# Kernel optimization log

Hardware: AMD Instinct MI355X
Metric: run time of the kernel (lower is better)

## Reference

```python
import jax, jax.numpy as jnp
import numpy as np

N_NODES = 50000
IN_FEATS, HID_FEATS, OUT_FEATS, HEADS = 128, 32, 64, 4
NEG_SLOPE = 0.2
EPS = 1e-16


def gat_conv(x, src, dst, W, att_src, att_dst, bias, heads, out_ch, concat):
    """PyG-style GATConv. src/dst: [E] (self-loops already included).
    W: [in, heads*out_ch]; att_src/att_dst: [heads, out_ch]; bias: [heads*out_ch] or [out_ch].
    """
    n = x.shape[0]
    xw = (x @ W).reshape(n, heads, out_ch)                     # [N,H,C]
    a_src = (xw * att_src).sum(-1)                             # [N,H]
    a_dst = (xw * att_dst).sum(-1)                             # [N,H]
    e = jax.nn.leaky_relu(a_src[src] + a_dst[dst], NEG_SLOPE)  # [E,H]
    # segment softmax over incoming edges of each destination node
    m = jax.ops.segment_max(e, dst, num_segments=n)
    e = jnp.exp(e - m[dst])
    denom = jax.ops.segment_sum(e, dst, num_segments=n)
    alpha = e / (denom[dst] + EPS)                             # [E,H]
    out = jax.ops.segment_sum(alpha[:, :, None] * xw[src], dst, num_segments=n)  # [N,H,C]
    out = out.reshape(n, heads * out_ch) if concat else out.mean(axis=1)
    return out + bias


def setup_inputs() -> dict:
    key = jax.random.key(0)
    ks = jax.random.split(key, 10)
    E = 1600000
    x = jax.random.normal(ks[0], (N_NODES, IN_FEATS), dtype=jnp.float32)
    edge_index = jax.random.randint(ks[1], (2, E), 0, N_NODES, dtype=jnp.int64)
    s1 = 1.0 / np.sqrt(IN_FEATS)
    W1 = jax.random.uniform(ks[2], (IN_FEATS, HEADS * HID_FEATS), jnp.float32, -s1, s1)
    att_src1 = jax.random.normal(ks[3], (HEADS, HID_FEATS), dtype=jnp.float32) * 0.1
    att_dst1 = jax.random.normal(ks[4], (HEADS, HID_FEATS), dtype=jnp.float32) * 0.1
    b1 = jnp.zeros((HEADS * HID_FEATS,), jnp.float32)
    s2 = 1.0 / np.sqrt(HEADS * HID_FEATS)
    W2 = jax.random.uniform(ks[5], (HEADS * HID_FEATS, OUT_FEATS), jnp.float32, -s2, s2)
    att_src2 = jax.random.normal(ks[6], (1, OUT_FEATS), dtype=jnp.float32) * 0.1
    att_dst2 = jax.random.normal(ks[7], (1, OUT_FEATS), dtype=jnp.float32) * 0.1
    b2 = jnp.zeros((OUT_FEATS,), jnp.float32)
    return {"x": x, "edge_index": edge_index, "W1": W1, "att_src1": att_src1,
            "att_dst1": att_dst1, "b1": b1, "W2": W2, "att_src2": att_src2,
            "att_dst2": att_dst2, "b2": b2}


def reference(x, edge_index, W1, att_src1, att_dst1, b1, W2, att_src2, att_dst2, b2):
    n = x.shape[0]
    loops = jnp.arange(n, dtype=edge_index.dtype)
    src = jnp.concatenate([edge_index[0], loops])
    dst = jnp.concatenate([edge_index[1], loops])
    h = gat_conv(x, src, dst, W1, att_src1, att_dst1, b1, HEADS, HID_FEATS, True)
    h = jax.nn.elu(h)
    h = gat_conv(h, src, dst, W2, att_src2, att_dst2, b2, 1, OUT_FEATS, False)
    return h.mean(axis=0)
```

## Files before the change

### kernel.cpp

```cpp
#include <hip/hip_runtime.h>
#include <math.h>

#define N_NODES 50000
#define E_RAW   1600000
#define TE      (E_RAW + N_NODES)
#define TEP     (TE + 8 * N_NODES)
#define F_IN    128
#define H1      4
#define F1      128
#define F2      64
#define NEG_SLOPE 0.2f
#define EPS_F   1e-16f
#define XPAD    136

#define NBINS   196
#define NBLK_A  128
#define EPB     ((TE + NBLK_A - 1) / NBLK_A)
#define MM_BLOCKS (N_NODES / 16)

__device__ __forceinline__ float lrelu(float v) { return v > 0.f ? v : NEG_SLOPE * v; }

typedef float vf2 __attribute__((ext_vector_type(2)));
typedef short short8 __attribute__((ext_vector_type(8)));
typedef float f32x4 __attribute__((ext_vector_type(4)));

__device__ __forceinline__ unsigned short f2bf(float f) {
    unsigned u = __float_as_uint(f);
    return (unsigned short)((u + 0x7fffu + ((u >> 16) & 1u)) >> 16);
}
__device__ __forceinline__ float bf2f(unsigned short s) {
    return __uint_as_float(((unsigned)s) << 16);
}
__device__ __forceinline__ unsigned char f2fp8(float f) {
    int p = __builtin_amdgcn_cvt_pk_fp8_f32(f, f, 0, false);
    return (unsigned char)(p & 0xff);
}
__device__ __forceinline__ vf2 fp8pair2f(int u) {
    return __builtin_amdgcn_cvt_pk_f32_fp8(u, false);
}

__global__ __launch_bounds__(256) void k_prep(const float* __restrict__ W1,
                                              const float* __restrict__ W2,
                                              unsigned short* __restrict__ w1t,
                                              unsigned short* __restrict__ w2t) {
    int idx = blockIdx.x * 256 + threadIdx.x;
    if (idx < 16384) {
        int c = idx >> 7, k = idx & 127;
        w1t[idx] = f2bf(W1[k * F1 + c]);
    } else {
        int j = idx - 16384;
        int c = j >> 7, k = j & 127;
        w2t[j] = f2bf(W2[k * F2 + c]);
    }
}

__global__ __launch_bounds__(256) void k_l1_mm_hist(
    const float* __restrict__ x, const unsigned short* __restrict__ w1t,
    const float* __restrict__ atts, const float* __restrict__ attd,
    unsigned char* __restrict__ xwf8, float* __restrict__ a1s, float* __restrict__ a1d,
    const int* __restrict__ ei, int* __restrict__ cnt) {
    __shared__ __align__(16) unsigned short wls[F1 * XPAD];
    __shared__ __align__(16) unsigned short xs[16 * XPAD];
    const int t = threadIdx.x;
    if (blockIdx.x >= MM_BLOCKS) {
        int* hist = (int*)wls;
        const int blk = blockIdx.x - MM_BLOCKS;
        for (int i = t; i < NBINS; i += 256) hist[i] = 0;
        __syncthreads();
        const int e0 = blk * EPB, e1 = min(TE, e0 + EPB);
        for (int e = e0 + t; e < e1; e += 256) {
            int d = (e < E_RAW) ? ei[E_RAW + e] : (e - E_RAW);
            atomicAdd(&hist[d >> 8], 1);
        }
        __syncthreads();
        for (int i = t; i < NBINS; i += 256) cnt[i * NBLK_A + blk] = hist[i];
        return;
    }
    const int n0 = blockIdx.x * 16;
    {
        const float4* src = (const float4*)(x + (size_t)n0 * F_IN);
#pragma unroll
        for (int i = 0; i < 2; ++i) {
            int idx = t + 256 * i;
            float4 v = src[idx];
            int row = idx >> 5;
            int col = (idx & 31) * 4;
            ushort4 o = { f2bf(v.x), f2bf(v.y), f2bf(v.z), f2bf(v.w) };
            *(ushort4*)(xs + row * XPAD + col) = o;
        }
        const uint4* wsrc = (const uint4*)w1t;
#pragma unroll
        for (int i = 0; i < 8; ++i) {
            int idx = t + 256 * i;
            uint4 v = wsrc[idx];
            int row = idx >> 4;
            int col = (idx & 15) * 8;
            *(uint4*)(wls + row * XPAD + col) = v;
        }
    }
    __syncthreads();
    const int w = t >> 6;
    const int lane = t & 63;
    const int quad = lane >> 4;
    const int ncol = lane & 15;
    const int ch0 = w * 32;
    const unsigned short* arow = xs + ncol * XPAD;
    const unsigned short* brow0 = wls + (ch0 + ncol) * XPAD;
    const unsigned short* brow1 = brow0 + 16 * XPAD;
    f32x4 acc0 = {0.f, 0.f, 0.f, 0.f}, acc1 = {0.f, 0.f, 0.f, 0.f};
#pragma unroll
    for (int s = 0; s < 4; ++s) {
        int kb = s * 32 + quad * 8;
        short8 a  = *(const short8*)(arow + kb);
        short8 b0 = *(const short8*)(brow0 + kb);
        short8 b1 = *(const short8*)(brow1 + kb);
        acc0 = __builtin_amdgcn_mfma_f32_16x16x32_bf16(a, b0, acc0, 0, 0, 0);
        acc1 = __builtin_amdgcn_mfma_f32_16x16x32_bf16(a, b1, acc1, 0, 0, 0);
    }
    const int ch = ch0 + ncol;
    const float as0 = atts[ch], as1 = atts[ch + 16];
    const float ad0 = attd[ch], ad1 = attd[ch + 16];
#pragma unroll
    for (int reg = 0; reg < 4; ++reg) {
        const int n = n0 + quad * 4 + reg;
        float v0 = acc0[reg], v1 = acc1[reg];
        xwf8[(size_t)n * F1 + ch] = f2fp8(v0);
        xwf8[(size_t)n * F1 + ch + 16] = f2fp8(v1);
        float ps = fmaf(v0, as0, v1 * as1);
        float pd = fmaf(v0, ad0, v1 * ad1);
#pragma unroll
        for (int off = 1; off < 16; off <<= 1) {
            ps += __shfl_xor(ps, off);
            pd += __shfl_xor(pd, off);
        }
        if (ncol == 0) {
            a1s[n * H1 + w] = ps;
            a1d[n * H1 + w] = pd;
        }
    }
}

__global__ __launch_bounds__(64) void k_btot(int* __restrict__ cnt, int* __restrict__ btot) {
    const int bin = blockIdx.x, lane = threadIdx.x;
    int c0 = cnt[bin * NBLK_A + 2 * lane];
    int c1 = cnt[bin * NBLK_A + 2 * lane + 1];
    int s = c0 + c1;
    int incl = s;
#pragma unroll
    for (int off = 1; off < 64; off <<= 1) {
        int u = __shfl_up(incl, off, 64);
        if (lane >= off) incl += u;
    }
    int excl = incl - s;
    cnt[bin * NBLK_A + 2 * lane] = excl;
    cnt[bin * NBLK_A + 2 * lane + 1] = excl + c0;
    if (lane == 63) btot[bin] = incl;
}

__global__ __launch_bounds__(64) void k_bstart(const int* __restrict__ btot,
                                               int* __restrict__ bstart) {
    const int lane = threadIdx.x;
    int v[4]; int s = 0;
#pragma unroll
    for (int j = 0; j < 4; ++j) {
        int i = 4 * lane + j;
        v[j] = (i < NBINS) ? btot[i] : 0;
        s += v[j];
    }
    int incl = s;
#pragma unroll
    for (int off = 1; off < 64; off <<= 1) {
        int u = __shfl_up(incl, off, 64);
        if (lane >= off) incl += u;
    }
    int run = incl - s;
#pragma unroll
    for (int j = 0; j < 4; ++j) {
        int i = 4 * lane + j;
        if (i < NBINS) bstart[i] = run;
        run += v[j];
    }
    if (lane == 63) bstart[NBINS] = TE;
}

__global__ __launch_bounds__(256) void k_scatter_coarse(const int* __restrict__ ei,
                                                        const int* __restrict__ cnt,
                                                        const int* __restrict__ bstart,
                                                        unsigned* __restrict__ cbuf) {
    __shared__ int cur[NBINS];
    const int t = threadIdx.x, blk = blockIdx.x;
    for (int i = t; i < NBINS; i += 256) cur[i] = cnt[i * NBLK_A + blk] + bstart[i];
    __syncthreads();
    const int e0 = blk * EPB, e1 = min(TE, e0 + EPB);
    for (int e = e0 + t; e < e1; e += 256) {
        int s, d;
        if (e < E_RAW) { s = ei[e]; d = ei[E_RAW + e]; }
        else { s = e - E_RAW; d = s; }
        int pos = atomicAdd(&cur[d >> 8], 1);
        cbuf[pos] = ((unsigned)(d & 255) << 16) | (unsigned)s;
    }
}

__global__ __launch_bounds__(256) void k_fine_hist(const unsigned* __restrict__ cbuf,
                                                   const int* __restrict__ bstart,
                                                   int* __restrict__ deg) {
    __shared__ int hist[256];
    const int t = threadIdx.x, b = blockIdx.x;
    hist[t] = 0;
    __syncthreads();
    const int i0 = bstart[b], i1 = bstart[b + 1];
    for (int i = i0 + t; i < i1; i += 256) atomicAdd(&hist[cbuf[i] >> 16], 1);
    __syncthreads();
    const int d = b * 256 + t;
    if (d < N_NODES) deg[d] = hist[t];
}

__global__ __launch_bounds__(1024) void k_scan1(const int* __restrict__ deg,
                                                int* __restrict__ incl, int* __restrict__ bsum) {
    int t = threadIdx.x, g = blockIdx.x;
    int idx = g * 1024 + t;
    int v = (idx < N_NODES) ? ((deg[idx] + 7) & ~7) : 0;
    int lane = t & 63, w = t >> 6;
#pragma unroll
    for (int off = 1; off < 64; off <<= 1) {
        int u = __shfl_up(v, off, 64);
        if (lane >= off) v += u;
    }
    __shared__ int ws[16];
    if (lane == 63) ws[w] = v;
    __syncthreads();
    if (w == 0 && lane < 16) {
        int s = ws[lane];
#pragma unroll
        for (int off = 1; off < 16; off <<= 1) {
            int u = __shfl_up(s, off, 16);
            if (lane >= off) s += u;
        }
        ws[lane] = s;
    }
    __syncthreads();
    if (w > 0) v += ws[w - 1];
    if (idx < N_NODES) incl[idx] = v;
    if (t == 1023) bsum[g] = v;
}

__global__ void k_scan2(int* __restrict__ bsum, int nblk) {
    int t = threadIdx.x;
    int v = (t < nblk) ? bsum[t] : 0;
#pragma unroll
    for (int off = 1; off < 64; off <<= 1) {
        int u = __shfl_up(v, off, 64);
        if (t >= off) v += u;
    }
    if (t < nblk) bsum[t] = v;
}

__global__ __launch_bounds__(1024) void k_scan3(const int* __restrict__ incl,
                                                const int* __restrict__ bsum,
                                                int* __restrict__ rowstart) {
    int idx = blockIdx.x * 1024 + threadIdx.x;
    if (idx >= N_NODES) return;
    int off = (blockIdx.x > 0) ? bsum[blockIdx.x - 1] : 0;
    rowstart[idx + 1] = incl[idx] + off;
    if (idx == 0) rowstart[0] = 0;
}

__global__ __launch_bounds__(256) void k_build_csr(const unsigned* __restrict__ cbuf,
                                                   const int* __restrict__ bstart,
                                                   const int* __restrict__ rowstart,
                                                   int* __restrict__ csr) {
    __shared__ int cur[256];
    const int t = threadIdx.x, b = blockIdx.x;
    const int d = b * 256 + t;
    cur[t] = (d < N_NODES) ? rowstart[d] : 0;
    __syncthreads();
    const int i0 = bstart[b], i1 = bstart[b + 1];
    for (int i = i0 + t; i < i1; i += 256) {
        unsigned v = cbuf[i];
        int pos = atomicAdd(&cur[v >> 16], 1);
        csr[pos] = (int)(v & 0xffffu);
    }
}

__global__ __launch_bounds__(256) void k_ew1(
    const int* __restrict__ rowstart, int* __restrict__ csr, const int* __restrict__ deg,
    const float* __restrict__ a1s, const float* __restrict__ a1d,
    unsigned short* __restrict__ ew1) {
    const int lane = threadIdx.x & 63;
    const int wid = threadIdx.x >> 6;
    const int n = blockIdx.x * 4 + wid;
    if (n >= N_NODES) return;
    const int rs = rowstart[n];
    const int dg = deg[n];
    const int re = rs + dg;
    const int re8 = rs + ((dg + 7) & ~7);
    const float4 ad = ((const float4*)a1d)[n];
    for (int i = rs + lane; i < re8; i += 64) {
        if (i < re) {
            int s = csr[i];
            float4 as = ((const float4*)a1s)[s];
            ew1[0 * TEP + i] = f2bf(expf(lrelu(as.x + ad.x)));
            ew1[1 * TEP + i] = f2bf(expf(lrelu(as.y + ad.y)));
            ew1[2 * TEP + i] = f2bf(expf(lrelu(as.z + ad.z)));
            ew1[3 * TEP + i] = f2bf(expf(lrelu(as.w + ad.w)));
        } else {
            csr[i] = 0;
            ew1[0 * TEP + i] = 0;
            ew1[1 * TEP + i] = 0;
            ew1[2 * TEP + i] = 0;
            ew1[3 * TEP + i] = 0;
        }
    }
}

__global__ __launch_bounds__(256) void k_l1_gather(
    const int* __restrict__ rowstart, const int* __restrict__ csr,
    const int* __restrict__ deg, const unsigned short* __restrict__ ew1,
    const unsigned short* __restrict__ xw8, const float* __restrict__ b1,
    float* __restrict__ h1) {
    const int lane = threadIdx.x & 63;
    const int wid = threadIdx.x >> 6;
    const int n = blockIdx.x * 4 + wid;
    if (n >= N_NODES) return;
    const int rs = rowstart[n];
    const int nb8 = (deg[n] + 7) >> 3;
    const int h = lane >> 4;
    const int4* c4 = (const int4*)(csr + rs);
    const ushort4* w4 = (const ushort4*)(ew1 + h * TEP + rs);
    float den = 0.f, ax = 0.f, ay = 0.f;
    for (int b = 0; b < nb8; ++b) {
        int4 sA = c4[2 * b], sB = c4[2 * b + 1];
        ushort4 wA = w4[2 * b], wB = w4[2 * b + 1];
        int u0 = xw8[sA.x * 64 + lane], u1 = xw8[sA.y * 64 + lane];
        int u2 = xw8[sA.z * 64 + lane], u3 = xw8[sA.w * 64 + lane];
        int u4 = xw8[sB.x * 64 + lane], u5 = xw8[sB.y * 64 + lane];
        int u6 = xw8[sB.z * 64 + lane], u7 = xw8[sB.w * 64 + lane];
        vf2 v0 = fp8pair2f(u0), v1 = fp8pair2f(u1), v2 = fp8pair2f(u2), v3 = fp8pair2f(u3);
        vf2 v4 = fp8pair2f(u4), v5 = fp8pair2f(u5), v6 = fp8pair2f(u6), v7 = fp8pair2f(u7);
        float wa0 = bf2f(wA.x), wa1 = bf2f(wA.y), wa2 = bf2f(wA.z), wa3 = bf2f(wA.w);
        float wb0 = bf2f(wB.x), wb1 = bf2f(wB.y), wb2 = bf2f(wB.z), wb3 = bf2f(wB.w);
        den += ((wa0 + wa1) + (wa2 + wa3)) + ((wb0 + wb1) + (wb2 + wb3));
        ax = fmaf(wa0, v0.x, fmaf(wa1, v1.x, fmaf(wa2, v2.x, fmaf(wa3, v3.x, ax))));
        ay = fmaf(wa0, v0.y, fmaf(wa1, v1.y, fmaf(wa2, v2.y, fmaf(wa3, v3.y, ay))));
        ax = fmaf(wb0, v4.x, fmaf(wb1, v5.x, fmaf(wb2, v6.x, fmaf(wb3, v7.x, ax))));
        ay = fmaf(wb0, v4.y, fmaf(wb1, v5.y, fmaf(wb2, v6.y, fmaf(wb3, v7.y, ay))));
    }
    const float inv = 1.f / (den + EPS_F);
    const int c0 = 2 * lane;
    float o0 = fmaf(ax, inv, b1[c0]);
    float o1 = fmaf(ay, inv, b1[c0 + 1]);
    o0 = o0 > 0.f ? o0 : expm1f(o0);
    o1 = o1 > 0.f ? o1 : expm1f(o1);
    ((float2*)h1)[(size_t)n * 64 + lane] = make_float2(o0, o1);
}

__global__ __launch_bounds__(256) void k_l2_mm(
    const float* __restrict__ h1, const unsigned short* __restrict__ w2t,
    const float* __restrict__ atts, const float* __restrict__ attd,
    unsigned char* __restrict__ xwf8, float* __restrict__ a2s, float* __restrict__ a2d) {
    __shared__ __align__(16) unsigned short wls[F2 * XPAD];
    __shared__ __align__(16) unsigned short xs[16 * XPAD];
    __shared__ float parts[16][4], partd[16][4];
    const int t = threadIdx.x;
    const int n0 = blockIdx.x * 16;
    {
        const float4* src = (const float4*)(h1 + (size_t)n0 * F1);
#pragma unroll
        for (int i = 0; i < 2; ++i) {
            int idx = t + 256 * i;
            float4 v = src[idx];
            int row = idx >> 5;
            int col = (idx & 31) * 4;
            ushort4 o = { f2bf(v.x), f2bf(v.y), f2bf(v.z), f2bf(v.w) };
            *(ushort4*)(xs + row * XPAD + col) = o;
        }
        const uint4* wsrc = (const uint4*)w2t;
#pragma unroll
        for (int i = 0; i < 4; ++i) {
            int idx = t + 256 * i;
            uint4 v = wsrc[idx];
            int row = idx >> 4;
            int col = (idx & 15) * 8;
            *(uint4*)(wls + row * XPAD + col) = v;
        }
    }
    __syncthreads();
    const int w = t >> 6;
    const int lane = t & 63;
    const int quad = lane >> 4;
    const int ncol = lane & 15;
    const int ch0 = w * 16;
    const unsigned short* arow = xs + ncol * XPAD;
    const unsigned short* brow = wls + (ch0 + ncol) * XPAD;
    f32x4 acc = {0.f, 0.f, 0.f, 0.f};
#pragma unroll
    for (int s = 0; s < 4; ++s) {
        int kb = s * 32 + quad * 8;
        short8 a = *(const short8*)(arow + kb);
        short8 b = *(const short8*)(brow + kb);
        acc = __builtin_amdgcn_mfma_f32_16x16x32_bf16(a, b, acc, 0, 0, 0);
    }
    const int ch = ch0 + ncol;
    const float asv = atts[ch], adv = attd[ch];
#pragma unroll
    for (int reg = 0; reg < 4; ++reg) {
        const int m = quad * 4 + reg;
        float v = acc[reg];
        xwf8[(size_t)(n0 + m) * F2 + ch] = f2fp8(v);
        float ps = v * asv, pd = v * adv;
#pragma unroll
        for (int off = 1; off < 16; off <<= 1) {
            ps += __shfl_xor(ps, off);
            pd += __shfl_xor(pd, off);
        }
        if (ncol == 0) { parts[m][w] = ps; partd[m][w] = pd; }
    }
    __syncthreads();
    if (t < 16) {
        a2s[n0 + t] = (parts[t][0] + parts[t][1]) + (parts[t][2] + parts[t][3]);
        a2d[n0 + t] = (partd[t][0] + partd[t][1]) + (partd[t][2] + partd[t][3]);
    }
}

__global__ __launch_bounds__(256) void k_ew2(
    const int* __restrict__ rowstart, const int* __restrict__ csr,
    const int* __restrict__ deg,
    const float* __restrict__ a2s, const float* __restrict__ a2d,
    unsigned short* __restrict__ ew2) {
    const int lane = threadIdx.x & 63;
    const int wid = threadIdx.x >> 6;
    const int n = blockIdx.x * 4 + wid;
    if (n >= N_NODES) return;
    const int rs = rowstart[n];
    const int dg = deg[n];
    const int re = rs + dg;
    const int re8 = rs + ((dg + 7) & ~7);
    const float adv = a2d[n];
    for (int i = rs + lane; i < re8; i += 64) {
        if (i < re) {
            int s = csr[i];
            ew2[i] = f2bf(expf(lrelu(a2s[s] + adv)));
        } else {
            ew2[i] = 0;
        }
    }
}

__global__ __launch_bounds__(256) void k_l2_gather(
    const int* __restrict__ rowstart, const int* __restrict__ csr,
    const int* __restrict__ deg, const unsigned short* __restrict__ ew2,
    const unsigned char* __restrict__ xw8, float* __restrict__ h2) {
    const int lane = threadIdx.x & 63;
    const int wid = threadIdx.x >> 6;
    const int n = blockIdx.x * 4 + wid;
    if (n >= N_NODES) return;
    const int rs = rowstart[n];
    const int nb8 = (deg[n] + 7) >> 3;
    const int4* c4 = (const int4*)(csr + rs);
    const ushort4* w4 = (const ushort4*)(ew2 + rs);
    float den = 0.f, acc = 0.f;
    for (int b = 0; b < nb8; ++b) {
        int4 sA = c4[2 * b], sB = c4[2 * b + 1];
        ushort4 wA = w4[2 * b], wB = w4[2 * b + 1];
        int u0 = xw8[(size_t)sA.x * F2 + lane], u1 = xw8[(size_t)sA.y * F2 + lane];
        int u2 = xw8[(size_t)sA.z * F2 + lane], u3 = xw8[(size_t)sA.w * F2 + lane];
        int u4 = xw8[(size_t)sB.x * F2 + lane], u5 = xw8[(size_t)sB.y * F2 + lane];
        int u6 = xw8[(size_t)sB.z * F2 + lane], u7 = xw8[(size_t)sB.w * F2 + lane];
        float v0 = fp8pair2f(u0).x, v1 = fp8pair2f(u1).x;
        float v2 = fp8pair2f(u2).x, v3 = fp8pair2f(u3).x;
        float v4 = fp8pair2f(u4).x, v5 = fp8pair2f(u5).x;
        float v6 = fp8pair2f(u6).x, v7 = fp8pair2f(u7).x;
        float wa0 = bf2f(wA.x), wa1 = bf2f(wA.y), wa2 = bf2f(wA.z), wa3 = bf2f(wA.w);
        float wb0 = bf2f(wB.x), wb1 = bf2f(wB.y), wb2 = bf2f(wB.z), wb3 = bf2f(wB.w);
        den += ((wa0 + wa1) + (wa2 + wa3)) + ((wb0 + wb1) + (wb2 + wb3));
        acc = fmaf(wa0, v0, fmaf(wa1, v1, fmaf(wa2, v2, fmaf(wa3, v3, acc))));
        acc = fmaf(wb0, v4, fmaf(wb1, v5, fmaf(wb2, v6, fmaf(wb3, v7, acc))));
    }
    h2[(size_t)n * F2 + lane] = acc / (den + EPS_F);
}

#define MEAN_BLOCKS 256
__global__ __launch_bounds__(256) void k_mean(const float* __restrict__ h2,
                                              double* __restrict__ accum) {
    const int t = threadIdx.x;
    const int c = t & 63;
    double acc = 0.0;
    const size_t total = (size_t)N_NODES * F2;
    for (size_t idx = (size_t)blockIdx.x * 256 + t; idx < total; idx += (size_t)MEAN_BLOCKS * 256)
        acc += (double)h2[idx];
    __shared__ double red[256];
    red[t] = acc;
    __syncthreads();
    if (t < 64) {
        double v = red[t] + red[t + 64] + red[t + 128] + red[t + 192];
        atomicAdd(&accum[c], v);
    }
}

__global__ void k_final(const double* __restrict__ accum, const float* __restrict__ b2,
                        float* __restrict__ out) {
    int t = threadIdx.x;
    if (t < F2) out[t] = (float)(accum[t] * (1.0 / (double)N_NODES)) + b2[t];
}

extern "C" void kernel_launch(void* const* d_in, const int* in_sizes, int n_in,
                              void* d_out, int out_size, void* d_ws, size_t ws_size,
                              hipStream_t stream) {
    (void)in_sizes; (void)n_in; (void)out_size; (void)ws_size;
    const float* x   = (const float*)d_in[0];
    const int*   ei  = (const int*)d_in[1];
    const float* W1  = (const float*)d_in[2];
    const float* as1 = (const float*)d_in[3];
    const float* ad1 = (const float*)d_in[4];
    const float* b1  = (const float*)d_in[5];
    const float* W2  = (const float*)d_in[6];
    const float* as2 = (const float*)d_in[7];
    const float* ad2 = (const float*)d_in[8];
    const float* b2  = (const float*)d_in[9];
    float* out = (float*)d_out;

    char* ws = (char*)d_ws;
    size_t off = 0;
    auto alloc = [&](size_t bytes) -> void* {
        void* p = ws + off;
        off += (bytes + 255) & ~(size_t)255;
        return p;
    };
    unsigned char*  xw1f8 = (unsigned char*)alloc((size_t)N_NODES * F1);
    float* h1       = (float*)alloc((size_t)N_NODES * F1 * 4);
    unsigned char*  xw2f8 = (unsigned char*)alloc((size_t)N_NODES * F2);
    float* h2       = (float*)alloc((size_t)N_NODES * F2 * 4);
    unsigned short* ew1 = (unsigned short*)alloc((size_t)H1 * TEP * 2);
    unsigned short* ew2 = (unsigned short*)alloc((size_t)TEP * 2);
    unsigned short* w1t = (unsigned short*)alloc((size_t)F1 * F1 * 2);
    unsigned short* w2t = (unsigned short*)alloc((size_t)F2 * F1 * 2);
    float* a1s      = (float*)alloc((size_t)N_NODES * H1 * 4);
    float* a1d      = (float*)alloc((size_t)N_NODES * H1 * 4);
    float* a2s      = (float*)alloc((size_t)N_NODES * 4);
    float* a2d      = (float*)alloc((size_t)N_NODES * 4);
    int*   deg      = (int*)alloc((size_t)N_NODES * 4);
    unsigned* cbuf  = (unsigned*)alloc((size_t)TE * 4);
    int*   cnt      = (int*)alloc((size_t)NBINS * NBLK_A * 4);
    int*   btot     = (int*)alloc((size_t)NBINS * 4);
    int*   bstart   = (int*)alloc((size_t)(NBINS + 1) * 4);
    int*   rowstart = (int*)alloc((size_t)(N_NODES + 1) * 4);
    int*   csr      = (int*)alloc((size_t)TEP * 4);
    int*   incl     = (int*)alloc((size_t)N_NODES * 4);
    int*   bsum     = (int*)alloc(64 * 4);
    double* accum   = (double*)alloc(F2 * 8);

    const int nscan = (N_NODES + 1023) / 1024;
    const int nwave4 = (N_NODES + 3) / 4;

    hipMemsetAsync(accum, 0, F2 * 8, stream);
    k_prep<<<96, 256, 0, stream>>>(W1, W2, w1t, w2t);
    k_l1_mm_hist<<<MM_BLOCKS + NBLK_A, 256, 0, stream>>>(x, w1t, as1, ad1, xw1f8, a1s, a1d, ei, cnt);
    k_btot<<<NBINS, 64, 0, stream>>>(cnt, btot);
    k_bstart<<<1, 64, 0, stream>>>(btot, bstart);
    k_scatter_coarse<<<NBLK_A, 256, 0, stream>>>(ei, cnt, bstart, cbuf);
    k_fine_hist<<<NBINS, 256, 0, stream>>>(cbuf, bstart, deg);
    k_scan1<<<nscan, 1024, 0, stream>>>(deg, incl, bsum);
    k_scan2<<<1, 64, 0, stream>>>(bsum, nscan);
    k_scan3<<<nscan, 1024, 0, stream>>>(incl, bsum, rowstart);
    k_build_csr<<<NBINS, 256, 0, stream>>>(cbuf, bstart, rowstart, csr);
    k_ew1<<<nwave4, 256, 0, stream>>>(rowstart, csr, deg, a1s, a1d, ew1);
    k_l1_gather<<<nwave4, 256, 0, stream>>>(rowstart, csr, deg, ew1,
                                            (const unsigned short*)xw1f8, b1, h1);
    k_l2_mm<<<MM_BLOCKS, 256, 0, stream>>>(h1, w2t, as2, ad2, xw2f8, a2s, a2d);
    k_ew2<<<nwave4, 256, 0, stream>>>(rowstart, csr, deg, a2s, a2d, ew2);
    k_l2_gather<<<nwave4, 256, 0, stream>>>(rowstart, csr, deg, ew2, xw2f8, h2);
    k_mean<<<MEAN_BLOCKS, 256, 0, stream>>>(h2, accum);
    k_final<<<1, 64, 0, stream>>>(accum, b2, out);
}
```

Baseline: 314.0 us.

## Fuse edge-weight computation into gather kernels with sentinel-node padding

Removes the separate k_ew1/k_ew2 kernels that wrote bf16 exp edge weights to global memory. The gathers now compute exp(leaky_relu(a_src+a_dst)) inline from the a_src values of each gathered neighbor. CSR rows are padded to multiples of 16 with a sentinel node whose a_src is -1e30, so padded edges get zero weight without branching. The gather lanes are also reorganised to load 4 fp8 features per lane and split the edges across half-waves or quarter-waves, followed by a shuffle reduction. This saves the edge-weight write and re-read traffic and two kernel launches. In exchange it recomputes exp per lane, issues extra a_src gathers, and pads rows more heavily.

```diff
diff --git a/kernel.cpp b/kernel.cpp
--- a/kernel.cpp
+++ b/kernel.cpp
@@ -2,9 +2,10 @@
 #include <math.h>
 
 #define N_NODES 50000
+#define SN      N_NODES
 #define E_RAW   1600000
 #define TE      (E_RAW + N_NODES)
-#define TEP     (TE + 8 * N_NODES)
+#define TEP     (TE + 16 * N_NODES)
 #define F_IN    128
 #define H1      4
 #define F1      128
@@ -28,21 +29,23 @@
     unsigned u = __float_as_uint(f);
     return (unsigned short)((u + 0x7fffu + ((u >> 16) & 1u)) >> 16);
 }
-__device__ __forceinline__ float bf2f(unsigned short s) {
-    return __uint_as_float(((unsigned)s) << 16);
-}
 __device__ __forceinline__ unsigned char f2fp8(float f) {
     int p = __builtin_amdgcn_cvt_pk_fp8_f32(f, f, 0, false);
     return (unsigned char)(p & 0xff);
 }
-__device__ __forceinline__ vf2 fp8pair2f(int u) {
-    return __builtin_amdgcn_cvt_pk_f32_fp8(u, false);
+__device__ __forceinline__ vf2 fp8lo(unsigned u) {
+    return __builtin_amdgcn_cvt_pk_f32_fp8((int)u, false);
+}
+__device__ __forceinline__ vf2 fp8hi(unsigned u) {
+    return __builtin_amdgcn_cvt_pk_f32_fp8((int)u, true);
 }
 
 __global__ __launch_bounds__(256) void k_prep(const float* __restrict__ W1,
                                               const float* __restrict__ W2,
                                               unsigned short* __restrict__ w1t,
-                                              unsigned short* __restrict__ w2t) {
+                                              unsigned short* __restrict__ w2t,
+                                              float* __restrict__ a1s,
+                                              float* __restrict__ a2s) {
     int idx = blockIdx.x * 256 + threadIdx.x;
     if (idx < 16384) {
         int c = idx >> 7, k = idx & 127;
@@ -52,6 +55,8 @@
         int c = j >> 7, k = j & 127;
         w2t[j] = f2bf(W2[k * F2 + c]);
     }
+    if (blockIdx.x == 0 && threadIdx.x < H1) a1s[SN * H1 + threadIdx.x] = -1e30f;
+    if (blockIdx.x == 0 && threadIdx.x == H1) a2s[SN] = -1e30f;
 }
 
 __global__ __launch_bounds__(256) void k_l1_mm_hist(
@@ -219,7 +224,7 @@
                                                 int* __restrict__ incl, int* __restrict__ bsum) {
     int t = threadIdx.x, g = blockIdx.x;
     int idx = g * 1024 + t;
-    int v = (idx < N_NODES) ? ((deg[idx] + 7) & ~7) : 0;
+    int v = (idx < N_NODES) ? ((deg[idx] + 15) & ~15) : 0;
     int lane = t & 63, w = t >> 6;
 #pragma unroll
     for (int off = 1; off < 64; off <<= 1) {
@@ -268,6 +273,7 @@
 __global__ __launch_bounds__(256) void k_build_csr(const unsigned* __restrict__ cbuf,
                                                    const int* __restrict__ bstart,
                                                    const int* __restrict__ rowstart,
+                                                   const int* __restrict__ deg,
                                                    int* __restrict__ csr) {
     __shared__ int cur[256];
     const int t = threadIdx.x, b = blockIdx.x;
@@ -280,78 +286,93 @@
         int pos = atomicAdd(&cur[v >> 16], 1);
         csr[pos] = (int)(v & 0xffffu);
     }
-}
-
-__global__ __launch_bounds__(256) void k_ew1(
-    const int* __restrict__ rowstart, int* __restrict__ csr, const int* __restrict__ deg,
-    const float* __restrict__ a1s, const float* __restrict__ a1d,
-    unsigned short* __restrict__ ew1) {
+    __syncthreads();
+    if (d < N_NODES) {
+        const int pend = rowstart[d] + ((deg[d] + 15) & ~15);
+        for (int i = cur[t]; i < pend; ++i) csr[i] = SN;
+    }
+}
+
+__global__ __launch_bounds__(256) void k_l1_gather(
+    const int* __restrict__ rowstart, const int* __restrict__ csr,
+    const int* __restrict__ deg, const float* __restrict__ a1s,
+    const float* __restrict__ a1d, const unsigned* __restrict__ xwu,
+    const float* __restrict__ b1, float* __restrict__ h1) {
     const int lane = threadIdx.x & 63;
     const int wid = threadIdx.x >> 6;
     const int n = blockIdx.x * 4 + wid;
     if (n >= N_NODES) return;
     const int rs = rowstart[n];
-    const int dg = deg[n];
-    const int re = rs + dg;
-    const int re8 = rs + ((dg + 7) & ~7);
-    const float4 ad = ((const float4*)a1d)[n];
-    for (int i = rs + lane; i < re8; i += 64) {
-        if (i < re) {
-            int s = csr[i];
-            float4 as = ((const float4*)a1s)[s];
-            ew1[0 * TEP + i] = f2bf(expf(lrelu(as.x + ad.x)));
-            ew1[1 * TEP + i] = f2bf(expf(lrelu(as.y + ad.y)));
-            ew1[2 * TEP + i] = f2bf(expf(lrelu(as.z + ad.z)));
-            ew1[3 * TEP + i] = f2bf(expf(lrelu(as.w + ad.w)));
-        } else {
-            csr[i] = 0;
-            ew1[0 * TEP + i] = 0;
-            ew1[1 * TEP + i] = 0;
-            ew1[2 * TEP + i] = 0;
-            ew1[3 * TEP + i] = 0;
-        }
-    }
-}
-
-__global__ __launch_bounds__(256) void k_l1_gather(
-    const int* __restrict__ rowstart, const int* __restrict__ csr,
-    const int* __restrict__ deg, const unsigned short* __restrict__ ew1,
-    const unsigned short* __restrict__ xw8, const float* __restrict__ b1,
-    float* __restrict__ h1) {
-    const int lane = threadIdx.x & 63;
-    const int wid = threadIdx.x >> 6;
-    const int n = blockIdx.x * 4 + wid;
-    if (n >= N_NODES) return;
-    const int rs = rowstart[n];
-    const int nb8 = (deg[n] + 7) >> 3;
-    const int h = lane >> 4;
+    const int nb16 = (deg[n] + 15) >> 4;
+    const int half = lane >> 5;
+    const int sub = lane & 31;
+    const int h = sub >> 3;
+    const float adh = a1d[n * H1 + h];
     const int4* c4 = (const int4*)(csr + rs);
-    const ushort4* w4 = (const ushort4*)(ew1 + h * TEP + rs);
-    float den = 0.f, ax = 0.f, ay = 0.f;
-    for (int b = 0; b < nb8; ++b) {
-        int4 sA = c4[2 * b], sB = c4[2 * b + 1];
-        ushort4 wA = w4[2 * b], wB = w4[2 * b + 1];
-        int u0 = xw8[sA.x * 64 + lane], u1 = xw8[sA.y * 64 + lane];
-        int u2 = xw8[sA.z * 64 + lane], u3 = xw8[sA.w * 64 + lane];
-        int u4 = xw8[sB.x * 64 + lane], u5 = xw8[sB.y * 64 + lane];
-        int u6 = xw8[sB.z * 64 + lane], u7 = xw8[sB.w * 64 + lane];
-        vf2 v0 = fp8pair2f(u0), v1 = fp8pair2f(u1), v2 = fp8pair2f(u2), v3 = fp8pair2f(u3);
-        vf2 v4 = fp8pair2f(u4), v5 = fp8pair2f(u5), v6 = fp8pair2f(u6), v7 = fp8pair2f(u7);
-        float wa0 = bf2f(wA.x), wa1 = bf2f(wA.y), wa2 = bf2f(wA.z), wa3 = bf2f(wA.w);
-        float wb0 = bf2f(wB.x), wb1 = bf2f(wB.y), wb2 = bf2f(wB.z), wb3 = bf2f(wB.w);
-        den += ((wa0 + wa1) + (wa2 + wa3)) + ((wb0 + wb1) + (wb2 + wb3));
-        ax = fmaf(wa0, v0.x, fmaf(wa1, v1.x, fmaf(wa2, v2.x, fmaf(wa3, v3.x, ax))));
-        ay = fmaf(wa0, v0.y, fmaf(wa1, v1.y, fmaf(wa2, v2.y, fmaf(wa3, v3.y, ay))));
-        ax = fmaf(wb0, v4.x, fmaf(wb1, v5.x, fmaf(wb2, v6.x, fmaf(wb3, v7.x, ax))));
-        ay = fmaf(wb0, v4.y, fmaf(wb1, v5.y, fmaf(wb2, v6.y, fmaf(wb3, v7.y, ay))));
-    }
-    const float inv = 1.f / (den + EPS_F);
-    const int c0 = 2 * lane;
-    float o0 = fmaf(ax, inv, b1[c0]);
-    float o1 = fmaf(ay, inv, b1[c0 + 1]);
-    o0 = o0 > 0.f ? o0 : expm1f(o0);
-    o1 = o1 > 0.f ? o1 : expm1f(o1);
-    ((float2*)h1)[(size_t)n * 64 + lane] = make_float2(o0, o1);
+    float den = 0.f, f0 = 0.f, f1 = 0.f, f2 = 0.f, f3 = 0.f;
+    for (int b = 0; b < nb16; ++b) {
+        const int i0 = 4 * b + 2 * half;
+        int4 sA = c4[i0], sB = c4[i0 + 1];
+        float as0 = a1s[sA.x * H1 + h], as1 = a1s[sA.y * H1 + h];
+        float as2 = a1s[sA.z * H1 + h], as3 = a1s[sA.w * H1 + h];
+        float as4 = a1s[sB.x * H1 + h], as5 = a1s[sB.y * H1 + h];
+        float as6 = a1s[sB.z * H1 + h], as7 = a1s[sB.w * H1 + h];
+        unsigned u0 = xwu[sA.x * 32 + sub], u1 = xwu[sA.y * 32 + sub];
+        unsigned u2 = xwu[sA.z * 32 + sub], u3 = xwu[sA.w * 32 + sub];
+        unsigned u4 = xwu[sB.x * 32 + sub], u5 = xwu[sB.y * 32 + sub];
+        unsigned u6 = xwu[sB.z * 32 + sub], u7 = xwu[sB.w * 32 + sub];
+        float w0 = __expf(lrelu(as0 + adh));
+        float w1 = __expf(lrelu(as1 + adh));
+        float w2 = __expf(lrelu(as2 + adh));
+        float w3 = __expf(lrelu(as3 + adh));
+        float w4 = __expf(lrelu(as4 + adh));
+        float w5 = __expf(lrelu(as5 + adh));
+        float w6 = __expf(lrelu(as6 + adh));
+        float w7 = __expf(lrelu(as7 + adh));
+        den += ((w0 + w1) + (w2 + w3)) + ((w4 + w5) + (w6 + w7));
+        vf2 l0 = fp8lo(u0), v0 = fp8hi(u0);
+        f0 = fmaf(w0, l0.x, f0); f1 = fmaf(w0, l0.y, f1);
+        f2 = fmaf(w0, v0.x, f2); f3 = fmaf(w0, v0.y, f3);
+        vf2 l1 = fp8lo(u1), v1 = fp8hi(u1);
+        f0 = fmaf(w1, l1.x, f0); f1 = fmaf(w1, l1.y, f1);
+        f2 = fmaf(w1, v1.x, f2); f3 = fmaf(w1, v1.y, f3);
+        vf2 l2 = fp8lo(u2), v2 = fp8hi(u2);
+        f0 = fmaf(w2, l2.x, f0); f1 = fmaf(w2, l2.y, f1);
+        f2 = fmaf(w2, v2.x, f2); f3 = fmaf(w2, v2.y, f3);
+        vf2 l3 = fp8lo(u3), v3 = fp8hi(u3);
+        f0 = fmaf(w3, l3.x, f0); f1 = fmaf(w3, l3.y, f1);
+        f2 = fmaf(w3, v3.x, f2); f3 = fmaf(w3, v3.y, f3);
+        vf2 l4 = fp8lo(u4), v4 = fp8hi(u4);
+        f0 = fmaf(w4, l4.x, f0); f1 = fmaf(w4, l4.y, f1);
+        f2 = fmaf(w4, v4.x, f2); f3 = fmaf(w4, v4.y, f3);
+        vf2 l5 = fp8lo(u5), v5 = fp8hi(u5);
+        f0 = fmaf(w5, l5.x, f0); f1 = fmaf(w5, l5.y, f1);
+        f2 = fmaf(w5, v5.x, f2); f3 = fmaf(w5, v5.y, f3);
+        vf2 l6 = fp8lo(u6), v6 = fp8hi(u6);
+        f0 = fmaf(w6, l6.x, f0); f1 = fmaf(w6, l6.y, f1);
+        f2 = fmaf(w6, v6.x, f2); f3 = fmaf(w6, v6.y, f3);
+        vf2 l7 = fp8lo(u7), v7 = fp8hi(u7);
+        f0 = fmaf(w7, l7.x, f0); f1 = fmaf(w7, l7.y, f1);
+        f2 = fmaf(w7, v7.x, f2); f3 = fmaf(w7, v7.y, f3);
+    }
+    f0 += __shfl_xor(f0, 32);
+    f1 += __shfl_xor(f1, 32);
+    f2 += __shfl_xor(f2, 32);
+    f3 += __shfl_xor(f3, 32);
+    den += __shfl_xor(den, 32);
+    if (half == 0) {
+        const float inv = 1.f / (den + EPS_F);
+        float4 bb = ((const float4*)b1)[sub];
+        float o0 = fmaf(f0, inv, bb.x);
+        float o1 = fmaf(f1, inv, bb.y);
+        float o2 = fmaf(f2, inv, bb.z);
+        float o3 = fmaf(f3, inv, bb.w);
+        o0 = o0 > 0.f ? o0 : expm1f(o0);
+        o1 = o1 > 0.f ? o1 : expm1f(o1);
+        o2 = o2 > 0.f ? o2 : expm1f(o2);
+        o3 = o3 > 0.f ? o3 : expm1f(o3);
+        ((float4*)h1)[(size_t)n * 32 + sub] = make_float4(o0, o1, o2, o3);
+    }
 }
 
 __global__ __launch_bounds__(256) void k_l2_mm(
@@ -422,61 +443,58 @@
     }
 }
 
-__global__ __launch_bounds__(256) void k_ew2(
+__global__ __launch_bounds__(256) void k_l2_gather(
     const int* __restrict__ rowstart, const int* __restrict__ csr,
-    const int* __restrict__ deg,
-    const float* __restrict__ a2s, const float* __restrict__ a2d,
-    unsigned short* __restrict__ ew2) {
+    const int* __restrict__ deg, const float* __restrict__ a2s,
+    const float* __restrict__ a2d, const unsigned* __restrict__ xwu,
+    float* __restrict__ h2) {
     const int lane = threadIdx.x & 63;
     const int wid = threadIdx.x >> 6;
     const int n = blockIdx.x * 4 + wid;
     if (n >= N_NODES) return;
     const int rs = rowstart[n];
-    const int dg = deg[n];
-    const int re = rs + dg;
-    const int re8 = rs + ((dg + 7) & ~7);
+    const int nb16 = (deg[n] + 15) >> 4;
+    const int q = lane >> 4;
+    const int sub = lane & 15;
     const float adv = a2d[n];
-    for (int i = rs + lane; i < re8; i += 64) {
-        if (i < re) {
-            int s = csr[i];
-            ew2[i] = f2bf(expf(lrelu(a2s[s] + adv)));
-        } else {
-            ew2[i] = 0;
-        }
-    }
-}
-
-__global__ __launch_bounds__(256) void k_l2_gather(
-    const int* __restrict__ rowstart, const int* __restrict__ csr,
-    const int* __restrict__ deg, const unsigned short* __restrict__ ew2,
-    const unsigned char* __restrict__ xw8, float* __restrict__ h2) {
-    const int lane = threadIdx.x & 63;
-    const int wid = threadIdx.x >> 6;
-    const int n = blockIdx.x * 4 + wid;
-    if (n >= N_NODES) return;
-    const int rs = rowstart[n];
-    const int nb8 = (deg[n] + 7) >> 3;
-    const int4* c4 = (const int4*)(csr + rs);
-    const ushort4* w4 = (const ushort4*)(ew2 + rs);
-    float den = 0.f, acc = 0.f;
-    for (int b = 0; b < nb8; ++b) {
-        int4 sA = c4[2 * b], sB = c4[2 * b + 1];
-        ushort4 wA = w4[2 * b], wB = w4[2 * b + 1];
-        int u0 = xw8[(size_t)sA.x * F2 + lane], u1 = xw8[(size_t)sA.y * F2 + lane];
-        int u2 = xw8[(size_t)sA.z * F2 + lane], u3 = xw8[(size_t)sA.w * F2 + lane];
-        int u4 = xw8[(size_t)sB.x * F2 + lane], u5 = xw8[(size_t)sB.y * F2 + lane];
-        int u6 = xw8[(size_t)sB.z * F2 + lane], u7 = xw8[(size_t)sB.w * F2 + lane];
-        float v0 = fp8pair2f(u0).x, v1 = fp8pair2f(u1).x;
-        float v2 = fp8pair2f(u2).x, v3 = fp8pair2f(u3).x;
-        float v4 = fp8pair2f(u4).x, v5 = fp8pair2f(u5).x;
-        float v6 = fp8pair2f(u6).x, v7 = fp8pair2f(u7).x;
-        float wa0 = bf2f(wA.x), wa1 = bf2f(wA.y), wa2 = bf2f(wA.z), wa3 = bf2f(wA.w);
-        float wb0 = bf2f(wB.x), wb1 = bf2f(wB.y), wb2 = bf2f(wB.z), wb3 = bf2f(wB.w);
-        den += ((wa0 + wa1) + (wa2 + wa3)) + ((wb0 + wb1) + (wb2 + wb3));
-        acc = fmaf(wa0, v0, fmaf(wa1, v1, fmaf(wa2, v2, fmaf(wa3, v3, acc))));
-        acc = fmaf(wb0, v4, fmaf(wb1, v5, fmaf(wb2, v6, fmaf(wb3, v7, acc))));
-    }
-    h2[(size_t)n * F2 + lane] = acc / (den + EPS_F);
+    float den = 0.f, f0 = 0.f, f1 = 0.f, f2 = 0.f, f3 = 0.f;
+    for (int b = 0; b < nb16; ++b) {
+        const int e = rs + 16 * b + q;
+        int s0 = csr[e], s1 = csr[e + 4], s2 = csr[e + 8], s3 = csr[e + 12];
+        float as0 = a2s[s0], as1 = a2s[s1], as2 = a2s[s2], as3 = a2s[s3];
+        unsigned u0 = xwu[s0 * 16 + sub], u1 = xwu[s1 * 16 + sub];
+        unsigned u2 = xwu[s2 * 16 + sub], u3 = xwu[s3 * 16 + sub];
+        float w0 = __expf(lrelu(as0 + adv));
+        float w1 = __expf(lrelu(as1 + adv));
+        float w2 = __expf(lrelu(as2 + adv));
+        float w3 = __expf(lrelu(as3 + adv));
+        den += (w0 + w1) + (w2 + w3);
+        vf2 l0 = fp8lo(u0), v0 = fp8hi(u0);
+        f0 = fmaf(w0, l0.x, f0); f1 = fmaf(w0, l0.y, f1);
+        f2 = fmaf(w0, v0.x, f2); f3 = fmaf(w0, v0.y, f3);
+        vf2 l1 = fp8lo(u1), v1 = fp8hi(u1);
+        f0 = fmaf(w1, l1.x, f0); f1 = fmaf(w1, l1.y, f1);
+        f2 = fmaf(w1, v1.x, f2); f3 = fmaf(w1, v1.y, f3);
+        vf2 l2 = fp8lo(u2), v2 = fp8hi(u2);
+        f0 = fmaf(w2, l2.x, f0); f1 = fmaf(w2, l2.y, f1);
+        f2 = fmaf(w2, v2.x, f2); f3 = fmaf(w2, v2.y, f3);
+        vf2 l3 = fp8lo(u3), v3 = fp8hi(u3);
+        f0 = fmaf(w3, l3.x, f0); f1 = fmaf(w3, l3.y, f1);
+        f2 = fmaf(w3, v3.x, f2); f3 = fmaf(w3, v3.y, f3);
+    }
+#pragma unroll
+    for (int off = 16; off <= 32; off <<= 1) {
+        f0 += __shfl_xor(f0, off);
+        f1 += __shfl_xor(f1, off);
+        f2 += __shfl_xor(f2, off);
+        f3 += __shfl_xor(f3, off);
+        den += __shfl_xor(den, off);
+    }
+    if (lane < 16) {
+        const float inv = 1.f / (den + EPS_F);
+        ((float4*)h2)[(size_t)n * 16 + sub] =
+            make_float4(f0 * inv, f1 * inv, f2 * inv, f3 * inv);
+    }
 }
 
 #define MEAN_BLOCKS 256
@@ -526,17 +544,15 @@
         off += (bytes + 255) & ~(size_t)255;
         return p;
     };
-    unsigned char*  xw1f8 = (unsigned char*)alloc((size_t)N_NODES * F1);
+    unsigned char*  xw1f8 = (unsigned char*)alloc((size_t)(N_NODES + 1) * F1);
     float* h1       = (float*)alloc((size_t)N_NODES * F1 * 4);
-    unsigned char*  xw2f8 = (unsigned char*)alloc((size_t)N_NODES * F2);
+    unsigned char*  xw2f8 = (unsigned char*)alloc((size_t)(N_NODES + 1) * F2);
     float* h2       = (float*)alloc((size_t)N_NODES * F2 * 4);
-    unsigned short* ew1 = (unsigned short*)alloc((size_t)H1 * TEP * 2);
-    unsigned short* ew2 = (unsigned short*)alloc((size_t)TEP * 2);
     unsigned short* w1t = (unsigned short*)alloc((size_t)F1 * F1 * 2);
     unsigned short* w2t = (unsigned short*)alloc((size_t)F2 * F1 * 2);
-    float* a1s      = (float*)alloc((size_t)N_NODES * H1 * 4);
+    float* a1s      = (float*)alloc((size_t)(N_NODES + 1) * H1 * 4);
     float* a1d      = (float*)alloc((size_t)N_NODES * H1 * 4);
-    float* a2s      = (float*)alloc((size_t)N_NODES * 4);
+    float* a2s      = (float*)alloc((size_t)(N_NODES + 1) * 4);
     float* a2d      = (float*)alloc((size_t)N_NODES * 4);
     int*   deg      = (int*)alloc((size_t)N_NODES * 4);
     unsigned* cbuf  = (unsigned*)alloc((size_t)TE * 4);
@@ -553,7 +569,7 @@
     const int nwave4 = (N_NODES + 3) / 4;
 
     hipMemsetAsync(accum, 0, F2 * 8, stream);
-    k_prep<<<96, 256, 0, stream>>>(W1, W2, w1t, w2t);
+    k_prep<<<96, 256, 0, stream>>>(W1, W2, w1t, w2t, a1s, a2s);
     k_l1_mm_hist<<<MM_BLOCKS + NBLK_A, 256, 0, stream>>>(x, w1t, as1, ad1, xw1f8, a1s, a1d, ei, cnt);
     k_btot<<<NBINS, 64, 0, stream>>>(cnt, btot);
     k_bstart<<<1, 64, 0, stream>>>(btot, bstart);
@@ -562,13 +578,12 @@
     k_scan1<<<nscan, 1024, 0, stream>>>(deg, incl, bsum);
     k_scan2<<<1, 64, 0, stream>>>(bsum, nscan);
     k_scan3<<<nscan, 1024, 0, stream>>>(incl, bsum, rowstart);
-    k_build_csr<<<NBINS, 256, 0, stream>>>(cbuf, bstart, rowstart, csr);
-    k_ew1<<<nwave4, 256, 0, stream>>>(rowstart, csr, deg, a1s, a1d, ew1);
-    k_l1_gather<<<nwave4, 256, 0, stream>>>(rowstart, csr, deg, ew1,
-                                            (const unsigned short*)xw1f8, b1, h1);
+    k_build_csr<<<NBINS, 256, 0, stream>>>(cbuf, bstart, rowstart, deg, csr);
+    k_l1_gather<<<nwave4, 256, 0, stream>>>(rowstart, csr, deg, a1s, a1d,
+                                            (const unsigned*)xw1f8, b1, h1);
     k_l2_mm<<<MM_BLOCKS, 256, 0, stream>>>(h1, w2t, as2, ad2, xw2f8, a2s, a2d);
-    k_ew2<<<nwave4, 256, 0, stream>>>(rowstart, csr, deg, a2s, a2d, ew2);
-    k_l2_gather<<<nwave4, 256, 0, stream>>>(rowstart, csr, deg, ew2, xw2f8, h2);
+    k_l2_gather<<<nwave4, 256, 0, stream>>>(rowstart, csr, deg, a2s, a2d,
+                                            (const unsigned*)xw2f8, h2);
     k_mean<<<MEAN_BLOCKS, 256, 0, stream>>>(h2, accum);
     k_final<<<1, 64, 0, stream>>>(accum, b2, out);
 }
```

After: 274.2 us. 1.15x faster.
